# Optimization experiments

Hardware: AMD Instinct MI355X
Metric: run time of the kernel (lower is better)

The kernel has to match this reference:

```python
import jax, jax.numpy as jnp
import numpy as np

EPS = 1e-12  # matches F.normalize default eps

def _l2_normalize(x, axis=-1):
    n = jnp.sqrt(jnp.sum(x * x, axis=axis, keepdims=True))
    return x / jnp.maximum(n, EPS)

def setup_inputs() -> dict:
    key = jax.random.key(0)
    k1, k2, k3 = jax.random.split(key, 3)
    B, C, D, V = 1024, 262144, 512, 512
    query = jax.random.normal(k1, (B, D), dtype=jnp.float32)
    keys = jax.random.normal(k2, (C, D), dtype=jnp.float32)
    values = jax.random.normal(k3, (C, V), dtype=jnp.float32)
    return {"query": query, "keys": keys, "values": values, "k": 8}

def reference(query, keys, values, k):
    # Cosine similarity: normalize both sides, then GEMM.
    q_norm = _l2_normalize(query, axis=1)          # [B, D]
    k_norm = _l2_normalize(keys, axis=1)           # [C, D]
    scores = jnp.matmul(q_norm, k_norm.T)          # [B, C]
    top_scores, top_indices = jax.lax.top_k(scores, k)  # [B, k] each
    # Vectorized gather replacing the per-row Python loop:
    retrieved_values = values[top_indices]         # [B, k, V]
    return retrieved_values, top_scores, top_indices
```

## Files before the change

kernel.cpp:

```cpp
#include <hip/hip_runtime.h>
#include <hip/hip_bf16.h>
#include <stdint.h>

#define B_Q   1024
#define C_K   262144
#define D_DIM 512
#define V_DIM 512
#define K_TOP 8
#define BM 128
#define BN 128
#define NT (C_K/BN)
#define TPB 32
#define CAP 2048
#define QS 8.0f
#define TAU_S 8.64f
#define RWIN 64
#define SC1 0x7F7F7F7F

typedef float f32x4  __attribute__((ext_vector_type(4)));
typedef float f32x16 __attribute__((ext_vector_type(16)));
typedef int   i32x8  __attribute__((ext_vector_type(8)));
typedef __attribute__((address_space(3))) unsigned char lds_uchar;
typedef __attribute__((address_space(1))) const unsigned char gbl_uchar;

__global__ __launch_bounds__(256) void pack_rows(const float* __restrict__ in,
                                                 uint8_t* __restrict__ outp,
                                                 int* cnt, int ncnt){
  if (cnt != nullptr && blockIdx.x == 0){
    for (int i = threadIdx.x; i < ncnt; i += 256) cnt[i] = 0;
  }
  __shared__ __align__(16) unsigned char stg[16384];
  const int tid  = threadIdx.x;
  const int w    = tid >> 6;
  const int lane = tid & 63;
  const int rt   = blockIdx.x;
  const int kt = lane >> 3, h = (lane >> 2) & 1, sub = (lane >> 1) & 1;
  const unsigned obase = (unsigned)kt*2048u + (unsigned)sub*1024u + (lane & 1)*8u;

  #pragma unroll
  for (int p=0; p<8; p++){
    const int r = p*4 + w;
    const float4* r4 = (const float4*)(in + ((size_t)rt*32 + r)*D_DIM);
    float4 a = r4[lane*2], b = r4[lane*2+1];
    float ss = a.x*a.x+a.y*a.y+a.z*a.z+a.w*a.w
             + b.x*b.x+b.y*b.y+b.z*b.z+b.w*b.w;
    #pragma unroll
    for (int off=32; off>0; off>>=1) ss += __shfl_xor(ss, off);
    float rn = QS / fmaxf(sqrtf(ss), 1e-12f);
    int w0 = __builtin_amdgcn_cvt_pk_fp8_f32(a.x*rn, a.y*rn, 0,  false);
    w0     = __builtin_amdgcn_cvt_pk_fp8_f32(a.z*rn, a.w*rn, w0, true);
    int w1 = __builtin_amdgcn_cvt_pk_fp8_f32(b.x*rn, b.y*rn, 0,  false);
    w1     = __builtin_amdgcn_cvt_pk_fp8_f32(b.z*rn, b.w*rn, w1, true);
    *(uint2*)(stg + obase + (unsigned)(r + 32*h)*16u) =
        make_uint2((unsigned)w0, (unsigned)w1);
  }
  __syncthreads();
  uint4* g = (uint4*)(outp + (size_t)rt*16384u);
  const uint4* s4 = (const uint4*)stg;
  #pragma unroll
  for (int p=0; p<4; p++) g[tid + p*256] = s4[tid + p*256];
}

__global__ __launch_bounds__(512) void gemm_topk(const uint8_t* __restrict__ qp,
                                                 const uint8_t* __restrict__ kp,
                                                 int* __restrict__ cnt,
                                                 float2* __restrict__ cand){
  extern __shared__ __align__(16) unsigned char alds[];

  const int tid  = threadIdx.x;
  const int lane = tid & 63;
  const int w    = tid >> 6;
  const int wm = w >> 2, wn = w & 3;

  const unsigned bid = blockIdx.x;
  const int xcd  = bid & 7;
  const int s    = bid >> 3;
  const int mt   = s & 7;
  const int nt0  = xcd*256 + (s >> 3)*TPB;

  #pragma unroll
  for (int i=0; i<8; i++)
    __builtin_amdgcn_global_load_lds(
        (gbl_uchar*)(qp + (size_t)mt*65536u + tid*16 + i*8192),
        (lds_uchar*)(alds + tid*16 + i*8192), 16, 0, 0);
  __syncthreads();

  f32x16 acc0 = {0}, acc1 = {0};
  union frag8 { uint4 q[2]; i32x8 v; };

  const uint8_t* bptr = kp + ((size_t)(nt0*4 + wn)*8)*2048 + (unsigned)lane*16u;
  uint4 pf0 = *(const uint4*)(bptr);
  uint4 pf1 = *(const uint4*)(bptr + 1024);

  const unsigned aoffA = (unsigned)(wm*16)*2048u + (unsigned)lane*16u;

  #define EPILOG(accR_, mh_) do{                                                \
    const int rbase = mt*BM + wm*64 + (mh_)*32 + 4*(lane>>5);                    \
    _Pragma("unroll")                                                            \
    for (int qd=0; qd<4; qd++){                                                  \
      float v0=(accR_)[qd*4+0], v1=(accR_)[qd*4+1];                              \
      float v2=(accR_)[qd*4+2], v3=(accR_)[qd*4+3];                              \
      float mx = fmaxf(fmaxf(v0,v1), fmaxf(v2,v3));                              \
      if (mx > TAU_S){                                                           \
        _Pragma("unroll")                                                        \
        for (int jj=0; jj<4; jj++){                                              \
          float v = (accR_)[qd*4+jj];                                            \
          if (v > TAU_S){                                                        \
            int rowg = rbase + jj + 8*qd;                                        \
            int pos = atomicAdd(cnt + rowg, 1);                                  \
            if (pos < CAP)                                                       \
              cand[(size_t)rowg*CAP + pos] = make_float2(v, __int_as_float(colg)); \
          }                                                                      \
        }                                                                        \
      }                                                                          \
    }                                                                            \
  }while(0)

  for (int t=0; t<TPB; t++){
    #pragma unroll
    for (int k8=0; k8<8; k8++){
      const bool last = (t == TPB-1) && (k8 == 7);
      const uint8_t* bnext = bptr + (k8 == 7 ? 25*2048 : 2048);
      uint4 nf0, nf1;
      if (!last){
        nf0 = *(const uint4*)(bnext);
        nf1 = *(const uint4*)(bnext + 1024);
      }
      frag8 fa0, fa1, fb;
      const unsigned ao = aoffA + (unsigned)k8*2048u;
      fa0.q[0] = *(const uint4*)(alds + ao);
      fa0.q[1] = *(const uint4*)(alds + ao + 1024u);
      fa1.q[0] = *(const uint4*)(alds + ao + 16384u);
      fa1.q[1] = *(const uint4*)(alds + ao + 16384u + 1024u);
      fb.q[0] = pf0; fb.q[1] = pf1;
      __builtin_amdgcn_s_setprio(1);
      acc0 = __builtin_amdgcn_mfma_scale_f32_32x32x64_f8f6f4(
                 fa0.v, fb.v, acc0, 0, 0, 0, SC1, 0, SC1);
      acc1 = __builtin_amdgcn_mfma_scale_f32_32x32x64_f8f6f4(
                 fa1.v, fb.v, acc1, 0, 0, 0, SC1, 0, SC1);
      __builtin_amdgcn_s_setprio(0);
      pf0 = nf0; pf1 = nf1;
      bptr = bnext;
    }

    {
      const int ntc  = nt0 + t;
      const int colg = ntc*BN + wn*32 + (lane&31);
      EPILOG(acc0, 0);
      EPILOG(acc1, 1);
      acc0 = (f32x16){0}; acc1 = (f32x16){0};
    }
  }
  #undef EPILOG
}

__global__ __launch_bounds__(256) void merge_rescore(const int* __restrict__ cnt,
                                                     const float2* __restrict__ cand,
                                                     const float* __restrict__ q,
                                                     const float* __restrict__ keys,
                                                     const float* __restrict__ values,
                                                     float* __restrict__ out){
  const int qi = blockIdx.x, tid = threadIdx.x;
  const int lane = tid & 63, w = tid >> 6;
  __shared__ __align__(16) float qrow[D_DIM];
  __shared__ __align__(16) float2 ent[CAP];
  __shared__ int    widx[RWIN];
  __shared__ double dsc[RWIN];
  __shared__ double wq[4];
  __shared__ int    fidx[8];
  __shared__ double fsc[8];

  float2 qv = ((const float2*)(q + (size_t)qi*D_DIM))[tid];
  qrow[tid*2] = qv.x; qrow[tid*2+1] = qv.y;
  double pq = (double)qv.x*qv.x + (double)qv.y*qv.y;
  #pragma unroll
  for (int off=32; off>0; off>>=1) pq += __shfl_xor(pq, off);
  if (lane == 0) wq[w] = pq;

  const int n = min(cnt[qi], CAP);
  for (int i = tid; i < n; i += 256) ent[i] = cand[(size_t)qi*CAP + i];
  if (tid < RWIN) widx[tid] = -1;
  __syncthreads();
  double qq = wq[0]+wq[1]+wq[2]+wq[3];

  for (int e = tid; e < n; e += 256){
    float se = ent[e].x; int ce = __float_as_int(ent[e].y);
    int rank = 0;
    for (int jx = 0; jx < n; jx++){
      float sj = ent[jx].x; int cj = __float_as_int(ent[jx].y);
      rank += (sj > se) || (sj == se && cj < ce);
    }
    if (rank < RWIN) widx[rank] = ce;
  }
  __syncthreads();

  const int g = tid >> 2, sub = tid & 3;
  const int ki = widx[g];
  const int kis = (ki < 0) ? 0 : ki;
  const float4* kr4 = (const float4*)(keys + (size_t)kis*D_DIM);
  const float4* qr4 = (const float4*)qrow;
  double da = 0.0, dk = 0.0;
  for (int i=0;i<32;i++){
    float4 kv  = kr4[sub*32+i];
    float4 qv4 = qr4[sub*32+i];
    da += (double)qv4.x*kv.x + (double)qv4.y*kv.y + (double)qv4.z*kv.z + (double)qv4.w*kv.w;
    dk += (double)kv.x*kv.x + (double)kv.y*kv.y + (double)kv.z*kv.z + (double)kv.w*kv.w;
  }
  da += __shfl_down(da, 2, 4); da += __shfl_down(da, 1, 4);
  dk += __shfl_down(dk, 2, 4); dk += __shfl_down(dk, 1, 4);
  if (sub == 0){
    double nq = fmax(sqrt(qq), 1e-12);
    double nk = fmax(sqrt(dk), 1e-12);
    dsc[g] = (ki < 0) ? -1e300 : da/(nq*nk);
  }
  __syncthreads();

  if (tid == 0){
    for (int s=0; s<8; s++){
      double bs = -1e301; int bi = 0; int bx = 0x7fffffff;
      for (int c=0; c<RWIN; c++){
        double v = dsc[c]; int ix = widx[c];
        if (v > bs || (v == bs && ix >= 0 && ix < bx)){ bs = v; bi = c; bx = ix; }
      }
      fsc[s] = bs; fidx[s] = (bx == 0x7fffffff) ? 0 : bx;
      dsc[bi] = -1e302;
    }
  }
  __syncthreads();

  float* out_sc  = out + (size_t)B_Q*K_TOP*V_DIM;
  float* out_idx = out_sc + (size_t)B_Q*K_TOP;
  if (tid < 8){
    out_sc [qi*K_TOP + tid] = (float)fsc[tid];
    out_idx[qi*K_TOP + tid] = (float)fidx[tid];
  }
  #pragma unroll
  for (int s=0; s<8; s++){
    const float2* vr = (const float2*)(values + (size_t)fidx[s]*V_DIM);
    float2* orow = (float2*)(out + ((size_t)qi*K_TOP + s)*V_DIM);
    orow[tid] = vr[tid];
  }
}

extern "C" void kernel_launch(void* const* d_in, const int* in_sizes, int n_in,
                              void* d_out, int out_size, void* d_ws, size_t ws_size,
                              hipStream_t stream){
  const float* q      = (const float*)d_in[0];
  const float* keys   = (const float*)d_in[1];
  const float* values = (const float*)d_in[2];
  unsigned char* ws = (unsigned char*)d_ws;
  uint8_t* qp = (uint8_t*)ws;
  uint8_t* kp = qp + (size_t)B_Q*D_DIM;
  int*    cnt  = (int*)(ws + (size_t)(B_Q + C_K)*D_DIM);
  float2* cand = (float2*)(ws + (size_t)(B_Q + C_K)*D_DIM + 8192);
  float* out = (float*)d_out;

  hipFuncSetAttribute((const void*)gemm_topk,
                      hipFuncAttributeMaxDynamicSharedMemorySize, 65536);

  pack_rows<<<dim3(B_Q/32), dim3(256), 0, stream>>>(q, qp, cnt, B_Q);
  pack_rows<<<dim3(C_K/32), dim3(256), 0, stream>>>(keys, kp, nullptr, 0);
  gemm_topk<<<dim3(512), dim3(512), 65536, stream>>>(qp, kp, cnt, cand);
  merge_rescore<<<dim3(B_Q), dim3(256), 0, stream>>>(cnt, cand, q, keys, values, out);
}
```

Baseline: 428.5 us.

## Enlarge GEMM block tile to 256 rows with 2x2 MFMA per wave

```diff
diff --git a/kernel.cpp b/kernel.cpp
--- a/kernel.cpp
+++ b/kernel.cpp
@@ -7,10 +7,10 @@
 #define D_DIM 512
 #define V_DIM 512
 #define K_TOP 8
-#define BM 128
+#define BM 256
 #define BN 128
 #define NT (C_K/BN)
-#define TPB 32
+#define TPB 16
 #define CAP 2048
 #define QS 8.0f
 #define TAU_S 8.64f
@@ -70,88 +70,99 @@
   const int tid  = threadIdx.x;
   const int lane = tid & 63;
   const int w    = tid >> 6;
-  const int wm = w >> 2, wn = w & 3;
+  const int wm = w >> 1, wn = w & 1;
 
   const unsigned bid = blockIdx.x;
   const int xcd  = bid & 7;
   const int s    = bid >> 3;
-  const int mt   = s & 7;
-  const int nt0  = xcd*256 + (s >> 3)*TPB;
-
-  #pragma unroll
-  for (int i=0; i<8; i++)
+  const int mt   = s & 3;
+  const int nt0  = xcd*256 + (s >> 2)*TPB;
+
+  #pragma unroll
+  for (int i=0; i<16; i++)
     __builtin_amdgcn_global_load_lds(
-        (gbl_uchar*)(qp + (size_t)mt*65536u + tid*16 + i*8192),
+        (gbl_uchar*)(qp + (size_t)mt*131072u + tid*16 + i*8192),
         (lds_uchar*)(alds + tid*16 + i*8192), 16, 0, 0);
   __syncthreads();
 
-  f32x16 acc0 = {0}, acc1 = {0};
+  f32x16 acc00 = {0}, acc01 = {0}, acc10 = {0}, acc11 = {0};
   union frag8 { uint4 q[2]; i32x8 v; };
 
-  const uint8_t* bptr = kp + ((size_t)(nt0*4 + wn)*8)*2048 + (unsigned)lane*16u;
-  uint4 pf0 = *(const uint4*)(bptr);
-  uint4 pf1 = *(const uint4*)(bptr + 1024);
-
-  const unsigned aoffA = (unsigned)(wm*16)*2048u + (unsigned)lane*16u;
-
-  #define EPILOG(accR_, mh_) do{                                                \
-    const int rbase = mt*BM + wm*64 + (mh_)*32 + 4*(lane>>5);                    \
-    _Pragma("unroll")                                                            \
-    for (int qd=0; qd<4; qd++){                                                  \
-      float v0=(accR_)[qd*4+0], v1=(accR_)[qd*4+1];                              \
-      float v2=(accR_)[qd*4+2], v3=(accR_)[qd*4+3];                              \
-      float mx = fmaxf(fmaxf(v0,v1), fmaxf(v2,v3));                              \
-      if (mx > TAU_S){                                                           \
-        _Pragma("unroll")                                                        \
-        for (int jj=0; jj<4; jj++){                                              \
-          float v = (accR_)[qd*4+jj];                                            \
-          if (v > TAU_S){                                                        \
-            int rowg = rbase + jj + 8*qd;                                        \
-            int pos = atomicAdd(cnt + rowg, 1);                                  \
-            if (pos < CAP)                                                       \
-              cand[(size_t)rowg*CAP + pos] = make_float2(v, __int_as_float(colg)); \
-          }                                                                      \
-        }                                                                        \
-      }                                                                          \
-    }                                                                            \
+  const uint8_t* bb = kp + ((size_t)(nt0*4 + wn*2)*8)*2048 + (unsigned)lane*16u;
+  #define BADDR(s_) (bb + (size_t)((s_)>>3)*65536u + (unsigned)(((s_)&7)*2048u))
+
+  uint4 c0a, c0b, c0c, c0d;
+  uint4 c1a, c1b, c1c, c1d;
+  c0a = *(const uint4*)(BADDR(0));          c0b = *(const uint4*)(BADDR(0)+1024);
+  c0c = *(const uint4*)(BADDR(0)+16384);    c0d = *(const uint4*)(BADDR(0)+16384+1024);
+  c1a = *(const uint4*)(BADDR(1));          c1b = *(const uint4*)(BADDR(1)+1024);
+  c1c = *(const uint4*)(BADDR(1)+16384);    c1d = *(const uint4*)(BADDR(1)+16384+1024);
+
+  const unsigned aoff0 = (unsigned)(wm*2)*16384u + (unsigned)lane*16u;
+
+  #define EPILOG(accR_, mh_, colg_) do{                                          \
+    const int rbase = mt*BM + wm*64 + (mh_)*32 + 4*(lane>>5);                     \
+    _Pragma("unroll")                                                             \
+    for (int qd=0; qd<4; qd++){                                                   \
+      float v0=(accR_)[qd*4+0], v1=(accR_)[qd*4+1];                               \
+      float v2=(accR_)[qd*4+2], v3=(accR_)[qd*4+3];                               \
+      float mx = fmaxf(fmaxf(v0,v1), fmaxf(v2,v3));                               \
+      if (mx > TAU_S){                                                            \
+        _Pragma("unroll")                                                         \
+        for (int jj=0; jj<4; jj++){                                               \
+          float v = (accR_)[qd*4+jj];                                             \
+          if (v > TAU_S){                                                         \
+            int rowg = rbase + jj + 8*qd;                                         \
+            int pos = atomicAdd(cnt + rowg, 1);                                   \
+            if (pos < CAP)                                                        \
+              cand[(size_t)rowg*CAP + pos] = make_float2(v, __int_as_float(colg_)); \
+          }                                                                       \
+        }                                                                         \
+      }                                                                           \
+    }                                                                             \
   }while(0)
 
-  for (int t=0; t<TPB; t++){
-    #pragma unroll
-    for (int k8=0; k8<8; k8++){
-      const bool last = (t == TPB-1) && (k8 == 7);
-      const uint8_t* bnext = bptr + (k8 == 7 ? 25*2048 : 2048);
-      uint4 nf0, nf1;
-      if (!last){
-        nf0 = *(const uint4*)(bnext);
-        nf1 = *(const uint4*)(bnext + 1024);
-      }
-      frag8 fa0, fa1, fb;
-      const unsigned ao = aoffA + (unsigned)k8*2048u;
-      fa0.q[0] = *(const uint4*)(alds + ao);
-      fa0.q[1] = *(const uint4*)(alds + ao + 1024u);
-      fa1.q[0] = *(const uint4*)(alds + ao + 16384u);
-      fa1.q[1] = *(const uint4*)(alds + ao + 16384u + 1024u);
-      fb.q[0] = pf0; fb.q[1] = pf1;
-      __builtin_amdgcn_s_setprio(1);
-      acc0 = __builtin_amdgcn_mfma_scale_f32_32x32x64_f8f6f4(
-                 fa0.v, fb.v, acc0, 0, 0, 0, SC1, 0, SC1);
-      acc1 = __builtin_amdgcn_mfma_scale_f32_32x32x64_f8f6f4(
-                 fa1.v, fb.v, acc1, 0, 0, 0, SC1, 0, SC1);
-      __builtin_amdgcn_s_setprio(0);
-      pf0 = nf0; pf1 = nf1;
-      bptr = bnext;
+  #pragma unroll 8
+  for (int st=0; st<TPB*8; st++){
+    frag8 fa0, fa1, fb0, fb1;
+    const unsigned ao = aoff0 + (unsigned)(st&7)*2048u;
+    fa0.q[0] = *(const uint4*)(alds + ao);
+    fa0.q[1] = *(const uint4*)(alds + ao + 1024u);
+    fa1.q[0] = *(const uint4*)(alds + ao + 16384u);
+    fa1.q[1] = *(const uint4*)(alds + ao + 16384u + 1024u);
+    fb0.q[0] = c0a; fb0.q[1] = c0b;
+    fb1.q[0] = c0c; fb1.q[1] = c0d;
+    __builtin_amdgcn_s_setprio(1);
+    acc00 = __builtin_amdgcn_mfma_scale_f32_32x32x64_f8f6f4(
+                fa0.v, fb0.v, acc00, 0, 0, 0, SC1, 0, SC1);
+    acc01 = __builtin_amdgcn_mfma_scale_f32_32x32x64_f8f6f4(
+                fa0.v, fb1.v, acc01, 0, 0, 0, SC1, 0, SC1);
+    acc10 = __builtin_amdgcn_mfma_scale_f32_32x32x64_f8f6f4(
+                fa1.v, fb0.v, acc10, 0, 0, 0, SC1, 0, SC1);
+    acc11 = __builtin_amdgcn_mfma_scale_f32_32x32x64_f8f6f4(
+                fa1.v, fb1.v, acc11, 0, 0, 0, SC1, 0, SC1);
+    __builtin_amdgcn_s_setprio(0);
+    c0a = c1a; c0b = c1b; c0c = c1c; c0d = c1d;
+    const int sn = (st+2 < TPB*8) ? st+2 : TPB*8-1;
+    c1a = *(const uint4*)(BADDR(sn));
+    c1b = *(const uint4*)(BADDR(sn) + 1024);
+    c1c = *(const uint4*)(BADDR(sn) + 16384);
+    c1d = *(const uint4*)(BADDR(sn) + 16384 + 1024);
+
+    if ((st&7) == 7){
+      const int ntc  = nt0 + (st>>3);
+      const int cg0  = ntc*BN + wn*64 + (lane&31);
+      const int cg1  = cg0 + 32;
+      EPILOG(acc00, 0, cg0);
+      EPILOG(acc01, 0, cg1);
+      EPILOG(acc10, 1, cg0);
+      EPILOG(acc11, 1, cg1);
+      acc00 = (f32x16){0}; acc01 = (f32x16){0};
+      acc10 = (f32x16){0}; acc11 = (f32x16){0};
     }
-
-    {
-      const int ntc  = nt0 + t;
-      const int colg = ntc*BN + wn*32 + (lane&31);
-      EPILOG(acc0, 0);
-      EPILOG(acc1, 1);
-      acc0 = (f32x16){0}; acc1 = (f32x16){0};
-    }
   }
   #undef EPILOG
+  #undef BADDR
 }
 
 __global__ __launch_bounds__(256) void merge_rescore(const int* __restrict__ cnt,
@@ -256,10 +267,10 @@
   float* out = (float*)d_out;
 
   hipFuncSetAttribute((const void*)gemm_topk,
-                      hipFuncAttributeMaxDynamicSharedMemorySize, 65536);
+                      hipFuncAttributeMaxDynamicSharedMemorySize, 131072);
 
   pack_rows<<<dim3(B_Q/32), dim3(256), 0, stream>>>(q, qp, cnt, B_Q);
   pack_rows<<<dim3(C_K/32), dim3(256), 0, stream>>>(keys, kp, nullptr, 0);
-  gemm_topk<<<dim3(512), dim3(512), 65536, stream>>>(qp, kp, cnt, cand);
+  gemm_topk<<<dim3(512), dim3(512), 131072, stream>>>(qp, kp, cnt, cand);
   merge_rescore<<<dim3(B_Q), dim3(256), 0, stream>>>(cnt, cand, q, keys, values, out);
 }
```

Measured after the change: 903.5 us. 2.11x slower.
